# Optimization experiments

Hardware: AMD Instinct MI355X
Metric: run time of the kernel (lower is better)

Reference implementation:

```python
import jax, jax.numpy as jnp
import numpy as np

N, D, K = 32768, 128, 16
EPS = 1e-8  # torch cosine_similarity eps


def setup_inputs() -> dict:
    key = jax.random.key(0)
    k1, k2, kW1, kW2, kV = jax.random.split(key, 5)
    # xavier_normal std for [K, fan_in, fan_out]-style tensors (torch treats dim0 as batch? no:
    # xavier_normal_ on a 3D tensor uses fan_in = D*1? torch computes fan from dims 1.. with receptive field.
    # fan_in = size(1)*rf, fan_out = size(0)*rf where rf = prod(shape[2:]).
    def xavier_std(shape):
        rf = int(np.prod(shape[2:])) if len(shape) > 2 else 1
        fan_in = shape[1] * rf
        fan_out = shape[0] * rf
        return float(np.sqrt(2.0 / (fan_in + fan_out)))
    W1 = jax.random.normal(kW1, (K, D, D), jnp.float32) * xavier_std((K, D, D))
    W2 = jax.random.normal(kW2, (K, D, D), jnp.float32) * xavier_std((K, D, D))
    V = jax.random.normal(kV, (K, 2 * D, 1), jnp.float32) * xavier_std((K, 2 * D, 1))
    b = jnp.zeros((K,), jnp.float32)
    x_1 = jax.random.normal(k1, (N, D), jnp.float32)
    x_2 = jax.random.normal(k2, (N, D), jnp.float32)
    return {"x_1": x_1, "x_2": x_2, "W1": W1, "W2": W2, "V": V, "b": b}


def reference(x_1, x_2, W1, W2, V, b):
    # Batched version of the per-slice loop: one bmm per side instead of K matmuls.
    x1_t = jnp.einsum('nd,kde->kne', x_1, W1)  # [K, N, D]
    x2_t = jnp.einsum('nd,kde->kne', x_2, W2)  # [K, N, D]
    # torch.cosine_similarity(dim=-1): dot / (clamp(||a||, eps) * clamp(||b||, eps))
    num = jnp.sum(x1_t * x2_t, axis=-1)                      # [K, N]
    n1 = jnp.maximum(jnp.sqrt(jnp.sum(x1_t * x1_t, -1)), EPS)
    n2 = jnp.maximum(jnp.sqrt(jnp.sum(x2_t * x2_t, -1)), EPS)
    part1 = num / (n1 * n2)                                  # [K, N]
    x_cat = jnp.concatenate([x_1, x_2], axis=-1)             # [N, 2D]
    part2 = jnp.einsum('nc,kc->kn', x_cat, V[:, :, 0])       # [K, N]
    fea = part1 + part2 + b[:, None]                         # [K, N]
    return jax.nn.relu(fea.T)                                # [N, K]
```

## Files before the change

### kernel.cpp

```cpp
#include <hip/hip_runtime.h>


typedef __attribute__((ext_vector_type(8))) __bf16 bf16x8;
typedef __attribute__((ext_vector_type(8))) unsigned short us8;
typedef __attribute__((ext_vector_type(4))) float f32x4;

static __device__ __forceinline__ unsigned short f2bf(float f) {
  unsigned u = __float_as_uint(f);
  u += 0x7FFFu + ((u >> 16) & 1u);
  return (unsigned short)(u >> 16);
}

static __device__ __forceinline__ bf16x8 as_bf(us8 u) {
  bf16x8 r;
  __builtin_memcpy(&r, &u, sizeof(r));
  return r;
}

__global__ void ntn_prep(const float* __restrict__ W1, const float* __restrict__ W2,
                         const float* __restrict__ V,
                         unsigned short* __restrict__ wsW, unsigned short* __restrict__ wsV) {
  const int t = threadIdx.x;
  const int blk = blockIdx.x;
  if (blk == 64) {
    if (t < 128) {
#pragma unroll
      for (int ui = 0; ui < 4; ++ui) {
        int u = ui * 128 + t;
        int lane = u & 63, cs = u >> 6;
        int q = lane >> 4, l15 = lane & 15;
        const float* src = V + l15 * 256 + cs * 32 + q * 8;
        us8 r;
#pragma unroll
        for (int j = 0; j < 8; ++j) r[j] = f2bf(src[j]);
        *(us8*)(wsV + (size_t)u * 8) = r;
      }
    }
    return;
  }

  __shared__ float T[128 * 68];
  const int k = blk >> 2, side = (blk >> 1) & 1, h = blk & 1;
  const float* W = (side ? W2 : W1) + k * 16384 + h * 64;

#pragma unroll
  for (int i = 0; i < 8; ++i) {
    int fidx = i * 256 + t;
    int d = fidx >> 4, c4 = fidx & 15;
    float4 v = *(const float4*)(W + d * 128 + c4 * 4);
    *(float4*)&T[d * 68 + c4 * 4] = v;
  }
  __syncthreads();

#pragma unroll
  for (int ui = 0; ui < 4; ++ui) {
    int u = ui * 256 + t;
    int lane = u & 63, s = (u >> 6) & 3, et2f = (u >> 8) & 3;
    int q = lane >> 4, l15 = lane & 15;
    int d0 = s * 32 + q * 8;
    int el = et2f * 16 + l15;
    us8 r;
#pragma unroll
    for (int j = 0; j < 8; ++j) r[j] = f2bf(T[(d0 + j) * 68 + el]);
    int cc = k * 4 + h * 2 + (et2f >> 1);
    int uic = side * 512 + (et2f & 1) * 256 + s * 64 + lane;
    *(us8*)(wsW + ((size_t)cc * 1024 + uic) * 8) = r;
  }
}

__global__ __launch_bounds__(256, 2) void ntn_main(
    const float* __restrict__ x1, const float* __restrict__ x2,
    const float* __restrict__ b,
    const unsigned short* __restrict__ wsW, const unsigned short* __restrict__ wsV,
    float* __restrict__ out) {
  __shared__ uint4 ldsW[2][1024];

  const int tid = threadIdx.x;
  const int lane = tid & 63, wave = tid >> 6;
  const int q = lane >> 4, l15 = lane & 15;
  const int kh = blockIdx.x & 3;
  const int rb = blockIdx.x >> 2;
  const int rowbase = rb * 128 + wave * 32;

  const f32x4 zero4 = {0.f, 0.f, 0.f, 0.f};

  auto stage = [&](int cc, int slot) {
    const unsigned short* src = wsW + (size_t)cc * 8192 + (size_t)(wave * 256 + lane) * 8;
    uint4* dst = &ldsW[slot][wave * 256];
#pragma unroll
    for (int i = 0; i < 4; ++i)
      __builtin_amdgcn_global_load_lds(
          (__attribute__((address_space(1))) void*)(void*)(src + i * 512),
          (__attribute__((address_space(3))) void*)(dst + i * 64), 16, 0, 0);
  };

  const int cbase = kh * 16;
  stage(cbase, 0);

  bf16x8 xb[2][2][4];
#pragma unroll
  for (int side = 0; side < 2; ++side) {
    const float* xp0 = side ? x2 : x1;
#pragma unroll
    for (int nt = 0; nt < 2; ++nt) {
#pragma unroll
      for (int s = 0; s < 4; ++s) {
        const float* p = xp0 + (size_t)(rowbase + nt * 16 + l15) * 128 + s * 32 + q * 8;
        float4 v0 = *(const float4*)p;
        float4 v1 = *(const float4*)(p + 4);
        us8 uu;
        uu[0] = f2bf(v0.x); uu[1] = f2bf(v0.y); uu[2] = f2bf(v0.z); uu[3] = f2bf(v0.w);
        uu[4] = f2bf(v1.x); uu[5] = f2bf(v1.y); uu[6] = f2bf(v1.z); uu[7] = f2bf(v1.w);
        xb[side][nt][s] = as_bf(uu);
      }
    }
  }

  f32x4 accP[2];
  {
    float4 bv = *(const float4*)(b + q * 4);
#pragma unroll
    for (int nt = 0; nt < 2; ++nt) {
      f32x4 a = zero4;
#pragma unroll
      for (int cs = 0; cs < 8; ++cs) {
        bf16x8 vf = as_bf(*(const us8*)(wsV + (size_t)(cs * 64 + lane) * 8));
        a = __builtin_amdgcn_mfma_f32_16x16x32_bf16(vf, xb[cs >> 2][nt][cs & 3], a, 0, 0, 0);
      }
      a.x += bv.x; a.y += bv.y; a.z += bv.z; a.w += bv.w;
      accP[nt] = a;
    }
  }

  float nm[2] = {0.f, 0.f}, q1[2] = {0.f, 0.f}, q2[2] = {0.f, 0.f};

  auto compute = [&](int slot) {
#pragma unroll
    for (int et = 0; et < 2; ++et) {
      bf16x8 wa[4], wb[4];
#pragma unroll
      for (int s = 0; s < 4; ++s) {
        wa[s] = as_bf(*(const us8*)&ldsW[slot][et * 256 + s * 64 + lane]);
        wb[s] = as_bf(*(const us8*)&ldsW[slot][512 + et * 256 + s * 64 + lane]);
      }
#pragma unroll
      for (int nt = 0; nt < 2; ++nt) {
        f32x4 a1 = zero4, a2 = zero4;
#pragma unroll
        for (int s = 0; s < 4; ++s)
          a1 = __builtin_amdgcn_mfma_f32_16x16x32_bf16(wa[s], xb[0][nt][s], a1, 0, 0, 0);
#pragma unroll
        for (int s = 0; s < 4; ++s)
          a2 = __builtin_amdgcn_mfma_f32_16x16x32_bf16(wb[s], xb[1][nt][s], a2, 0, 0, 0);
        nm[nt] += a1.x * a2.x + a1.y * a2.y + a1.z * a2.z + a1.w * a2.w;
        q1[nt] += a1.x * a1.x + a1.y * a1.y + a1.z * a1.z + a1.w * a1.w;
        q2[nt] += a2.x * a2.x + a2.y * a2.y + a2.z * a2.z + a2.w * a2.w;
      }
    }
  };

#pragma unroll 1
  for (int kk = 0; kk < 4; ++kk) {
#pragma unroll
    for (int q4 = 0; q4 < 4; ++q4) {
      const int c = kk * 4 + q4;
      __syncthreads();
      if (c < 15) stage(cbase + c + 1, (c + 1) & 1);
      compute(c & 1);
    }

    const int k = kh * 4 + kk;
#pragma unroll
    for (int nt = 0; nt < 2; ++nt) {
      float n = nm[nt], s1 = q1[nt], s2 = q2[nt];
      n  += __shfl_xor(n, 16);  n  += __shfl_xor(n, 32);
      s1 += __shfl_xor(s1, 16); s1 += __shfl_xor(s1, 32);
      s2 += __shfl_xor(s2, 16); s2 += __shfl_xor(s2, 32);
      float d1 = fmaxf(sqrtf(s1), 1e-8f);
      float d2 = fmaxf(sqrtf(s2), 1e-8f);
      float p1 = n / (d1 * d2);
      float pc = (kk == 0) ? accP[nt].x : (kk == 1) ? accP[nt].y
               : (kk == 2) ? accP[nt].z : accP[nt].w;
      if (q == kh)
        out[(size_t)(rowbase + nt * 16 + l15) * 16 + k] = fmaxf(p1 + pc, 0.f);
      nm[nt] = 0.f; q1[nt] = 0.f; q2[nt] = 0.f;
    }
  }
}

extern "C" void kernel_launch(void* const* d_in, const int* in_sizes, int n_in,
                              void* d_out, int out_size, void* d_ws, size_t ws_size,
                              hipStream_t stream) {
  const float* x1 = (const float*)d_in[0];
  const float* x2 = (const float*)d_in[1];
  const float* W1 = (const float*)d_in[2];
  const float* W2 = (const float*)d_in[3];
  const float* V  = (const float*)d_in[4];
  const float* b  = (const float*)d_in[5];
  float* out = (float*)d_out;
  unsigned short* wsW = (unsigned short*)d_ws;
  unsigned short* wsV = wsW + (size_t)65536 * 8;

  ntn_prep<<<65, 256, 0, stream>>>(W1, W2, V, wsW, wsV);
  ntn_main<<<1024, 256, 0, stream>>>(x1, x2, b, wsW, wsV, out);
}
```

Measured before the change: 128.1 us.

## Switch to 32x32 MFMA tiles and split linear term into separate kernel

Replaces the 16x16x32 MFMA tiling with 32x32x16 MFMA, so each wave covers 64 rows with larger accumulators, and rearranges the prepacked weight layout in the prep kernel to match. The V-projection plus bias moves into a separate ntn_part2 kernel that writes the output first. The main kernel then read-modify-writes each output entry to add the cosine term and apply ReLU. Grid size halves, launch bounds change to one block per CU, and register pressure rises. The extra kernel launch and output round trip add cost.

Result: slower. 146.6 us (+14.4%).

```diff
diff --git a/kernel.cpp b/kernel.cpp
--- a/kernel.cpp
+++ b/kernel.cpp
@@ -3,7 +3,7 @@
 
 typedef __attribute__((ext_vector_type(8))) __bf16 bf16x8;
 typedef __attribute__((ext_vector_type(8))) unsigned short us8;
-typedef __attribute__((ext_vector_type(4))) float f32x4;
+typedef __attribute__((ext_vector_type(16))) float f32x16;
 
 static __device__ __forceinline__ unsigned short f2bf(float f) {
   unsigned u = __float_as_uint(f);
@@ -23,18 +23,22 @@
   const int t = threadIdx.x;
   const int blk = blockIdx.x;
   if (blk == 64) {
-    if (t < 128) {
-#pragma unroll
-      for (int ui = 0; ui < 4; ++ui) {
-        int u = ui * 128 + t;
-        int lane = u & 63, cs = u >> 6;
-        int q = lane >> 4, l15 = lane & 15;
-        const float* src = V + l15 * 256 + cs * 32 + q * 8;
-        us8 r;
+    const int lane = t & 63, hh = (t >> 5) & 1, l31 = t & 31;
+#pragma unroll
+    for (int ui = 0; ui < 4; ++ui) {
+      int u = ui * 256 + t;
+      int cs = u >> 6;
+      us8 r;
+      if (l31 < 16) {
+        const float* src = V + l31 * 256 + cs * 16 + hh * 8;
 #pragma unroll
         for (int j = 0; j < 8; ++j) r[j] = f2bf(src[j]);
-        *(us8*)(wsV + (size_t)u * 8) = r;
-      }
+      } else {
+#pragma unroll
+        for (int j = 0; j < 8; ++j) r[j] = 0;
+      }
+      (void)lane;
+      *(us8*)(wsV + (size_t)u * 8) = r;
     }
     return;
   }
@@ -55,34 +59,66 @@
 #pragma unroll
   for (int ui = 0; ui < 4; ++ui) {
     int u = ui * 256 + t;
-    int lane = u & 63, s = (u >> 6) & 3, et2f = (u >> 8) & 3;
-    int q = lane >> 4, l15 = lane & 15;
-    int d0 = s * 32 + q * 8;
-    int el = et2f * 16 + l15;
+    int lane = u & 63, s = (u >> 6) & 7, q4l = (u >> 9) & 1;
+    int hh = lane >> 5, l31 = lane & 31;
+    int d0 = s * 16 + hh * 8;
+    int el = q4l * 32 + l31;
     us8 r;
 #pragma unroll
     for (int j = 0; j < 8; ++j) r[j] = f2bf(T[(d0 + j) * 68 + el]);
-    int cc = k * 4 + h * 2 + (et2f >> 1);
-    int uic = side * 512 + (et2f & 1) * 256 + s * 64 + lane;
+    int cc = k * 4 + h * 2 + q4l;
+    int uic = side * 512 + s * 64 + lane;
     *(us8*)(wsW + ((size_t)cc * 1024 + uic) * 8) = r;
   }
 }
 
-__global__ __launch_bounds__(256, 2) void ntn_main(
+__global__ __launch_bounds__(256, 1) void ntn_part2(
     const float* __restrict__ x1, const float* __restrict__ x2,
-    const float* __restrict__ b,
-    const unsigned short* __restrict__ wsW, const unsigned short* __restrict__ wsV,
+    const float* __restrict__ b, const unsigned short* __restrict__ wsV,
     float* __restrict__ out) {
-  __shared__ uint4 ldsW[2][1024];
-
   const int tid = threadIdx.x;
   const int lane = tid & 63, wave = tid >> 6;
-  const int q = lane >> 4, l15 = lane & 15;
+  const int hh = lane >> 5, l31 = lane & 31;
+  const int rowbase = blockIdx.x * 256 + wave * 64;
+  const f32x16 zero16 = {0.f};
+
+#pragma unroll
+  for (int nt = 0; nt < 2; ++nt) {
+    const int row = rowbase + nt * 32 + l31;
+    f32x16 c = zero16;
+#pragma unroll
+    for (int cs = 0; cs < 16; ++cs) {
+      const float* xp = (cs < 8) ? (x1 + (size_t)row * 128 + cs * 16 + hh * 8)
+                                 : (x2 + (size_t)row * 128 + (cs - 8) * 16 + hh * 8);
+      float4 v0 = *(const float4*)xp;
+      float4 v1 = *(const float4*)(xp + 4);
+      us8 uu;
+      uu[0] = f2bf(v0.x); uu[1] = f2bf(v0.y); uu[2] = f2bf(v0.z); uu[3] = f2bf(v0.w);
+      uu[4] = f2bf(v1.x); uu[5] = f2bf(v1.y); uu[6] = f2bf(v1.z); uu[7] = f2bf(v1.w);
+      bf16x8 vf = as_bf(*(const us8*)(wsV + (size_t)(cs * 64 + lane) * 8));
+      c = __builtin_amdgcn_mfma_f32_32x32x16_bf16(vf, as_bf(uu), c, 0, 0, 0);
+    }
+#pragma unroll
+    for (int r = 0; r < 8; ++r) {
+      int k = (r & 3) + 8 * (r >> 2) + 4 * hh;
+      out[(size_t)row * 16 + k] = c[r] + b[k];
+    }
+  }
+}
+
+__global__ __launch_bounds__(256, 1) void ntn_main(
+    const float* __restrict__ x1, const float* __restrict__ x2,
+    const unsigned short* __restrict__ wsW, float* __restrict__ out) {
+  __shared__ uint4 ldsW[2][1024];
+
+  const int tid = threadIdx.x;
+  const int lane = tid & 63, wave = tid >> 6;
+  const int hh = lane >> 5, l31 = lane & 31;
   const int kh = blockIdx.x & 3;
   const int rb = blockIdx.x >> 2;
-  const int rowbase = rb * 128 + wave * 32;
-
-  const f32x4 zero4 = {0.f, 0.f, 0.f, 0.f};
+  const int rowbase = rb * 256 + wave * 64;
+
+  const f32x16 zero16 = {0.f};
 
   auto stage = [&](int cc, int slot) {
     const unsigned short* src = wsW + (size_t)cc * 8192 + (size_t)(wave * 256 + lane) * 8;
@@ -97,15 +133,15 @@
   const int cbase = kh * 16;
   stage(cbase, 0);
 
-  bf16x8 xb[2][2][4];
+  bf16x8 xb[2][2][8];
 #pragma unroll
   for (int side = 0; side < 2; ++side) {
     const float* xp0 = side ? x2 : x1;
 #pragma unroll
     for (int nt = 0; nt < 2; ++nt) {
 #pragma unroll
-      for (int s = 0; s < 4; ++s) {
-        const float* p = xp0 + (size_t)(rowbase + nt * 16 + l15) * 128 + s * 32 + q * 8;
+      for (int s = 0; s < 8; ++s) {
+        const float* p = xp0 + (size_t)(rowbase + nt * 32 + l31) * 128 + s * 16 + hh * 8;
         float4 v0 = *(const float4*)p;
         float4 v1 = *(const float4*)(p + 4);
         us8 uu;
@@ -116,46 +152,30 @@
     }
   }
 
-  f32x4 accP[2];
-  {
-    float4 bv = *(const float4*)(b + q * 4);
+  float nm[2] = {0.f, 0.f}, q1[2] = {0.f, 0.f}, q2[2] = {0.f, 0.f};
+
+  auto compute = [&](int slot) {
+    f32x16 a1[2] = {zero16, zero16}, a2[2] = {zero16, zero16};
+#pragma unroll
+    for (int s = 0; s < 8; ++s) {
+      bf16x8 wa = as_bf(*(const us8*)&ldsW[slot][s * 64 + lane]);
+      bf16x8 wb = as_bf(*(const us8*)&ldsW[slot][512 + s * 64 + lane]);
+#pragma unroll
+      for (int nt = 0; nt < 2; ++nt) {
+        a1[nt] = __builtin_amdgcn_mfma_f32_32x32x16_bf16(wa, xb[0][nt][s], a1[nt], 0, 0, 0);
+        a2[nt] = __builtin_amdgcn_mfma_f32_32x32x16_bf16(wb, xb[1][nt][s], a2[nt], 0, 0, 0);
+      }
+    }
 #pragma unroll
     for (int nt = 0; nt < 2; ++nt) {
-      f32x4 a = zero4;
-#pragma unroll
-      for (int cs = 0; cs < 8; ++cs) {
-        bf16x8 vf = as_bf(*(const us8*)(wsV + (size_t)(cs * 64 + lane) * 8));
-        a = __builtin_amdgcn_mfma_f32_16x16x32_bf16(vf, xb[cs >> 2][nt][cs & 3], a, 0, 0, 0);
-      }
-      a.x += bv.x; a.y += bv.y; a.z += bv.z; a.w += bv.w;
-      accP[nt] = a;
-    }
-  }
-
-  float nm[2] = {0.f, 0.f}, q1[2] = {0.f, 0.f}, q2[2] = {0.f, 0.f};
-
-  auto compute = [&](int slot) {
-#pragma unroll
-    for (int et = 0; et < 2; ++et) {
-      bf16x8 wa[4], wb[4];
-#pragma unroll
-      for (int s = 0; s < 4; ++s) {
-        wa[s] = as_bf(*(const us8*)&ldsW[slot][et * 256 + s * 64 + lane]);
-        wb[s] = as_bf(*(const us8*)&ldsW[slot][512 + et * 256 + s * 64 + lane]);
-      }
-#pragma unroll
-      for (int nt = 0; nt < 2; ++nt) {
-        f32x4 a1 = zero4, a2 = zero4;
-#pragma unroll
-        for (int s = 0; s < 4; ++s)
-          a1 = __builtin_amdgcn_mfma_f32_16x16x32_bf16(wa[s], xb[0][nt][s], a1, 0, 0, 0);
-#pragma unroll
-        for (int s = 0; s < 4; ++s)
-          a2 = __builtin_amdgcn_mfma_f32_16x16x32_bf16(wb[s], xb[1][nt][s], a2, 0, 0, 0);
-        nm[nt] += a1.x * a2.x + a1.y * a2.y + a1.z * a2.z + a1.w * a2.w;
-        q1[nt] += a1.x * a1.x + a1.y * a1.y + a1.z * a1.z + a1.w * a1.w;
-        q2[nt] += a2.x * a2.x + a2.y * a2.y + a2.z * a2.z + a2.w * a2.w;
-      }
+      float n = 0.f, s1 = 0.f, s2 = 0.f;
+#pragma unroll
+      for (int r = 0; r < 16; ++r) {
+        n  += a1[nt][r] * a2[nt][r];
+        s1 += a1[nt][r] * a1[nt][r];
+        s2 += a2[nt][r] * a2[nt][r];
+      }
+      nm[nt] += n; q1[nt] += s1; q2[nt] += s2;
     }
   };
 
@@ -173,16 +193,16 @@
 #pragma unroll
     for (int nt = 0; nt < 2; ++nt) {
       float n = nm[nt], s1 = q1[nt], s2 = q2[nt];
-      n  += __shfl_xor(n, 16);  n  += __shfl_xor(n, 32);
-      s1 += __shfl_xor(s1, 16); s1 += __shfl_xor(s1, 32);
-      s2 += __shfl_xor(s2, 16); s2 += __shfl_xor(s2, 32);
+      n  += __shfl_xor(n, 32);
+      s1 += __shfl_xor(s1, 32);
+      s2 += __shfl_xor(s2, 32);
       float d1 = fmaxf(sqrtf(s1), 1e-8f);
       float d2 = fmaxf(sqrtf(s2), 1e-8f);
       float p1 = n / (d1 * d2);
-      float pc = (kk == 0) ? accP[nt].x : (kk == 1) ? accP[nt].y
-               : (kk == 2) ? accP[nt].z : accP[nt].w;
-      if (q == kh)
-        out[(size_t)(rowbase + nt * 16 + l15) * 16 + k] = fmaxf(p1 + pc, 0.f);
+      if (hh == 0) {
+        float* po = out + (size_t)(rowbase + nt * 32 + l31) * 16 + k;
+        *po = fmaxf(*po + p1, 0.f);
+      }
       nm[nt] = 0.f; q1[nt] = 0.f; q2[nt] = 0.f;
     }
   }
@@ -202,5 +222,6 @@
   unsigned short* wsV = wsW + (size_t)65536 * 8;
 
   ntn_prep<<<65, 256, 0, stream>>>(W1, W2, V, wsW, wsV);
-  ntn_main<<<1024, 256, 0, stream>>>(x1, x2, b, wsW, wsV, out);
-}
+  ntn_part2<<<128, 256, 0, stream>>>(x1, x2, b, wsV, out);
+  ntn_main<<<512, 256, 0, stream>>>(x1, x2, wsW, out);
+}
```
